# Performance work log

Hardware: AMD Instinct MI355X
Metric: run time of the kernel (lower is better)

## Reference

```python
import math
import jax, jax.numpy as jnp
import numpy as np

B, T, E = 2, 2048, 1024
H, KV = 16, 4
D = E // H          # 64
G = H // KV         # 4 groups


def rotate_half(x):
    x1, x2 = jnp.split(x, 2, axis=-1)
    return jnp.concatenate([-x2, x1], axis=-1)


def setup_inputs() -> dict:
    key = jax.random.key(0)
    ks = jax.random.split(key, 12)
    query = jax.random.normal(ks[0], (B, T, E), jnp.float32)
    key_t = jax.random.normal(ks[1], (B, T, E), jnp.float32)
    value = jax.random.normal(ks[2], (B, T, E), jnp.float32)
    # RoPE tables: [T, D]
    inv_freq = 1.0 / (10000.0 ** (np.arange(0, D, 2, dtype=np.float32) / D))
    pos = np.arange(T, dtype=np.float32)
    freqs = np.outer(pos, inv_freq)                      # [T, D/2]
    emb = np.concatenate([freqs, freqs], axis=-1)        # [T, D]
    cos_emb = jnp.asarray(np.cos(emb), jnp.float32)
    sin_emb = jnp.asarray(np.sin(emb), jnp.float32)
    # causal mask [1,1,T,T], True = keep
    mask = jnp.tril(jnp.ones((T, T), bool))[None, None, :, :]
    s = 0.02
    Wq = jax.random.normal(ks[3], (E, H * D), jnp.float32) * s
    bq = jnp.zeros((H * D,), jnp.float32)
    Wk = jax.random.normal(ks[4], (E, KV * D), jnp.float32) * s
    bk = jnp.zeros((KV * D,), jnp.float32)
    Wv = jax.random.normal(ks[5], (E, KV * D), jnp.float32) * s
    bv = jnp.zeros((KV * D,), jnp.float32)
    Wo = jax.random.normal(ks[6], (E, E), jnp.float32) * s
    bo = jnp.zeros((E,), jnp.float32)
    return {"query": query, "key": key_t, "value": value,
            "cos_emb": cos_emb, "sin_emb": sin_emb, "mask": mask,
            "Wq": Wq, "bq": bq, "Wk": Wk, "bk": bk,
            "Wv": Wv, "bv": bv, "Wo": Wo, "bo": bo}


def reference(query, key, value, cos_emb, sin_emb, mask,
              Wq, bq, Wk, bk, Wv, bv, Wo, bo):
    Bq, Tq, _ = query.shape
    Tk = key.shape[1]
    q = (query @ Wq + bq).reshape(Bq, Tq, H, D)          # [B,Tq,H,D]
    k = (key @ Wk + bk).reshape(Bq, Tk, KV, D)           # [B,Tk,KV,D]
    v = (value @ Wv + bv).reshape(Bq, Tk, KV, D)
    # expand kv heads across groups (head h = kv*G + g, consecutive repeat)
    k = jnp.repeat(k, G, axis=2)                         # [B,Tk,H,D]
    v = jnp.repeat(v, G, axis=2)
    # RoPE (applied post-expansion, as in the original)
    cos = cos_emb[None, :, None, :]                      # [1,T,1,D]
    sin = sin_emb[None, :, None, :]
    q = q * cos[:, :Tq] + rotate_half(q) * sin[:, :Tq]
    k = k * cos[:, :Tk] + rotate_half(k) * sin[:, :Tk]
    scores = jnp.einsum('bqhd,bkhd->bhqk', q, k) / math.sqrt(D)
    scores = jnp.where(mask[:, :, :Tq, :Tk], scores, jnp.float32(-jnp.inf))
    probs = jax.nn.softmax(scores, axis=-1)              # [B,H,Tq,Tk]
    attn = jnp.einsum('bhqk,bkhd->bqhd', probs, v).reshape(Bq, Tq, E)
    return attn @ Wo + bo
```

## Files before the change

kernel.cpp:

```cpp
#include <hip/hip_runtime.h>
#include <hip/hip_bf16.h>

constexpr int Bc  = 2;
constexpr int Tc  = 2048;
constexpr int Ec  = 1024;
constexpr int Hc  = 16;
constexpr int KVc = 4;
constexpr int Dc  = 64;

typedef short bf16x8 __attribute__((ext_vector_type(8)));
typedef short short4v __attribute__((ext_vector_type(4)));
typedef float f32x4  __attribute__((ext_vector_type(4)));
typedef float f32x16 __attribute__((ext_vector_type(16)));
typedef int   i32x4  __attribute__((ext_vector_type(4)));

__device__ inline short f2bf_bits(float f) {
    union { __hip_bfloat16 h; short s; } u;
    u.h = __float2bfloat16(f);
    return u.s;
}

__device__ inline float bf2f(short s) {
    union { short s16; __hip_bfloat16 h; } u;
    u.s16 = s;
    return __bfloat162float(u.h);
}

__device__ inline unsigned pkbf(float a, float b) {
    union { __hip_bfloat162 h2; unsigned u; } u;
    u.h2 = __float22bfloat162_rn(float2{a, b});
    return u.u;
}

__device__ inline float fexp2(float x) { return __builtin_exp2f(x); }

__device__ inline void permswap(unsigned &a, unsigned &b) {
    asm volatile("v_permlane32_swap_b32 %0, %1" : "+v"(a), "+v"(b));
}

__device__ inline void gload16(const short* g, short* lds) {
    __builtin_amdgcn_global_load_lds(
        (const __attribute__((address_space(1))) unsigned int*)g,
        (__attribute__((address_space(3))) unsigned int*)lds,
        16, 0, 0);
}

__global__ __launch_bounds__(256) void conv3_f32_bf16(
    const float* __restrict__ q, const float* __restrict__ k,
    const float* __restrict__ v,
    short* __restrict__ Xq, short* __restrict__ Xk, short* __restrict__ Xv)
{
    const int range = blockIdx.x >> 12;
    const int sub   = blockIdx.x & 4095;
    const float* x = range == 0 ? q : (range == 1 ? k : v);
    short*       y = range == 0 ? Xq : (range == 1 ? Xk : Xv);
    int i = (sub * 256 + threadIdx.x) * 4;
    float4 vv = *reinterpret_cast<const float4*>(x + i);
    short4v o;
    o[0] = f2bf_bits(vv.x);
    o[1] = f2bf_bits(vv.y);
    o[2] = f2bf_bits(vv.z);
    o[3] = f2bf_bits(vv.w);
    *reinterpret_cast<short4v*>(y + i) = o;
}

__global__ __launch_bounds__(256) void transp_all(
    const float* __restrict__ Wq, const float* __restrict__ Wk,
    const float* __restrict__ Wv, const float* __restrict__ Wo,
    short* __restrict__ Wqt, short* __restrict__ Wkt,
    short* __restrict__ Wvt, short* __restrict__ Wot)
{
    __shared__ float tile[32][33];
    const int id = blockIdx.x;
    const float* W; short* Wt; int N, bx, by;
    if (id < 1024)      { W = Wq; Wt = Wqt; N = 1024; bx = id & 31;          by = id >> 5; }
    else if (id < 1280) { W = Wk; Wt = Wkt; N = 256;  bx = (id - 1024) & 7;  by = (id - 1024) >> 3; }
    else if (id < 1536) { W = Wv; Wt = Wvt; N = 256;  bx = (id - 1280) & 7;  by = (id - 1280) >> 3; }
    else                { W = Wo; Wt = Wot; N = 1024; bx = (id - 1536) & 31; by = (id - 1536) >> 5; }
    const int K = 1024;
    int nb = bx * 32, kb = by * 32;
    int tx = threadIdx.x & 31, ty = threadIdx.x >> 5;
    #pragma unroll
    for (int j = 0; j < 4; ++j)
        tile[ty + j * 8][tx] = W[(size_t)(kb + ty + j * 8) * N + nb + tx];
    __syncthreads();
    #pragma unroll
    for (int j = 0; j < 4; ++j)
        Wt[(size_t)(nb + ty + j * 8) * K + kb + tx] = f2bf_bits(tile[tx][ty + j * 8]);
}

#define GEMM_CORE(A_, Bt_, Kdim_)                                              \
    const int lane = threadIdx.x & 63;                                         \
    const int w    = threadIdx.x >> 6;                                         \
    const int wm   = w >> 1, wn = w & 1;                                       \
    const int rin  = lane >> 3;                                                \
    const int swc  = ((lane & 7) ^ rin) * 8;                                   \
    f32x4 acc[4][2] = {};                                                      \
    for (int k0 = 0; k0 < (Kdim_); k0 += 64) {                                 \
        _Pragma("unroll")                                                      \
        for (int i2 = 0; i2 < 4; ++i2) {                                       \
            const int r = w * 32 + i2 * 8;                                     \
            gload16((A_) + (size_t)(m0 + r + rin) * (Kdim_) + k0 + swc,        \
                    As + r * 64);                                              \
        }                                                                      \
        _Pragma("unroll")                                                      \
        for (int i2 = 0; i2 < 2; ++i2) {                                       \
            const int r = w * 16 + i2 * 8;                                     \
            gload16((Bt_) + (size_t)(n0 + r + rin) * (Kdim_) + k0 + swc,       \
                    Bs + r * 64);                                              \
        }                                                                      \
        __syncthreads();                                                       \
        _Pragma("unroll")                                                      \
        for (int ks = 0; ks < 2; ++ks) {                                       \
            bf16x8 af[4], bfr[2];                                              \
            _Pragma("unroll")                                                  \
            for (int mi = 0; mi < 4; ++mi) {                                   \
                int row = wm * 64 + mi * 16 + (lane & 15);                     \
                int sl  = (ks * 4 + (lane >> 4)) ^ (row & 7);                  \
                af[mi] = *reinterpret_cast<const bf16x8*>(As + row * 64 + sl * 8); \
            }                                                                  \
            _Pragma("unroll")                                                  \
            for (int ni = 0; ni < 2; ++ni) {                                   \
                int row = wn * 32 + ni * 16 + (lane & 15);                     \
                int sl  = (ks * 4 + (lane >> 4)) ^ (row & 7);                  \
                bfr[ni] = *reinterpret_cast<const bf16x8*>(Bs + row * 64 + sl * 8); \
            }                                                                  \
            _Pragma("unroll")                                                  \
            for (int mi = 0; mi < 4; ++mi)                                     \
                _Pragma("unroll")                                              \
                for (int ni = 0; ni < 2; ++ni)                                 \
                    acc[mi][ni] = __builtin_amdgcn_mfma_f32_16x16x32_bf16(     \
                        af[mi], bfr[ni], acc[mi][ni], 0, 0, 0);                \
        }                                                                      \
        __syncthreads();                                                       \
    }

__global__ __launch_bounds__(256) void gemm_qkv(
    const short* __restrict__ Xq, const short* __restrict__ Xk,
    const short* __restrict__ Xv,
    const short* __restrict__ Wqt, const short* __restrict__ Wkt,
    const short* __restrict__ Wvt,
    const float* __restrict__ bq, const float* __restrict__ bk,
    const float* __restrict__ bv,
    short* __restrict__ Qp, short* __restrict__ Kp, short* __restrict__ VTp)
{
    __shared__ short As[128 * 64];
    __shared__ short Bs[64 * 64];
    const int gid = blockIdx.x;
    const short *A, *Bt; const float* bias; int bx, by, mode;
    if (gid < 512)      { mode = 0; A = Xq; Bt = Wqt; bias = bq; bx = gid & 15;         by = gid >> 4; }
    else if (gid < 640) { mode = 1; A = Xk; Bt = Wkt; bias = bk; bx = (gid - 512) & 3;  by = (gid - 512) >> 2; }
    else                { mode = 2; A = Xv; Bt = Wvt; bias = bv; bx = (gid - 640) & 3;  by = (gid - 640) >> 2; }
    const int m0 = by * 128, n0 = bx * 64;

    GEMM_CORE(A, Bt, 1024)

    #pragma unroll
    for (int mi = 0; mi < 4; ++mi)
        #pragma unroll
        for (int ni = 0; ni < 2; ++ni) {
            int col = n0 + wn * 32 + ni * 16 + (lane & 15);
            float bv2 = bias[col];
            #pragma unroll
            for (int i = 0; i < 4; ++i) {
                int row = m0 + wm * 64 + mi * 16 + ((lane >> 4) * 4) + i;
                float v = acc[mi][ni][i] + bv2;
                if (mode == 0)
                    Qp[(size_t)row * 1024 + col] = f2bf_bits(v);
                else if (mode == 1)
                    Kp[(size_t)row * 256 + col] = f2bf_bits(v);
                else
                    VTp[(((size_t)(row >> 11) * 256 + col) << 11) + (row & 2047)]
                        = f2bf_bits(v);
            }
        }
}

__global__ __launch_bounds__(256) void gemm_o(
    const short* __restrict__ A, const short* __restrict__ Bt,
    const float* __restrict__ bias, float* __restrict__ C)
{
    __shared__ short As[128 * 64];
    __shared__ short Bs[64 * 64];
    const int m0 = blockIdx.y * 128, n0 = blockIdx.x * 64;

    GEMM_CORE(A, Bt, 1024)

    #pragma unroll
    for (int mi = 0; mi < 4; ++mi)
        #pragma unroll
        for (int ni = 0; ni < 2; ++ni) {
            int col = n0 + wn * 32 + ni * 16 + (lane & 15);
            float bv2 = bias[col];
            #pragma unroll
            for (int i = 0; i < 4; ++i) {
                int row = m0 + wm * 64 + mi * 16 + ((lane >> 4) * 4) + i;
                C[(size_t)row * 1024 + col] = acc[mi][ni][i] + bv2;
            }
        }
}

__global__ __launch_bounds__(256) void rope_merged(
    short* __restrict__ Qp, short* __restrict__ Kp,
    const float* __restrict__ cosE, const float* __restrict__ sinE)
{
    short* x; int hbits; float scale; int idx;
    if (blockIdx.x < 2048) {
        x = Qp; hbits = 4; scale = 0.125f * 1.44269504089f;
        idx = blockIdx.x * 256 + threadIdx.x;
    } else {
        x = Kp; hbits = 2; scale = 1.0f;
        idx = (blockIdx.x - 2048) * 256 + threadIdx.x;
    }
    int dq  = (idx & 7) * 4;
    int hh  = (idx >> 3) & ((1 << hbits) - 1);
    int row = idx >> (3 + hbits);
    int t   = row & (Tc - 1);
    float4 c4 = *reinterpret_cast<const float4*>(cosE + t * 64 + dq);
    float4 s4 = *reinterpret_cast<const float4*>(sinE + t * 64 + dq);
    size_t base = (size_t)row * (64 << hbits) + hh * 64 + dq;
    short4v a = *reinterpret_cast<const short4v*>(x + base);
    short4v b = *reinterpret_cast<const short4v*>(x + base + 32);
    short4v oa, ob;
    float c[4] = {c4.x, c4.y, c4.z, c4.w};
    float s[4] = {s4.x, s4.y, s4.z, s4.w};
    #pragma unroll
    for (int j = 0; j < 4; ++j) {
        float x1 = bf2f(a[j]), x2 = bf2f(b[j]);
        oa[j] = f2bf_bits((x1 * c[j] - x2 * s[j]) * scale);
        ob[j] = f2bf_bits((x2 * c[j] + x1 * s[j]) * scale);
    }
    *reinterpret_cast<short4v*>(x + base)      = oa;
    *reinterpret_cast<short4v*>(x + base + 32) = ob;
}

__global__ __launch_bounds__(256, 3) void flash_gqa8(
    const short* __restrict__ Q,
    const short* __restrict__ Kx,
    const short* __restrict__ VT,
    short* __restrict__ attn,
    short* __restrict__ PO,
    float* __restrict__ ML)
{
    __shared__ short smem[16384];

    const int lane = threadIdx.x & 63;
    const int w    = threadIdx.x >> 6;
    const int lo   = lane & 31;
    const int hi   = lane >> 5;

    const int L   = blockIdx.x;
    const int xcd = L & 7;
    const int j   = L >> 3;
    const int g   = j & 3;
    const int u   = 39 - (j >> 2);
    int qt = 0, rem = u;
    while (true) { int nc0 = (qt >> 2) + 1; if (rem < nc0) break; rem -= nc0; ++qt; }
    const int c  = rem;
    const int nc = (qt >> 2) + 1;
    const int b   = xcd >> 2;
    const int kvh = xcd & 3;
    const int h   = kvh * 4 + g;
    const int slot = (b * 16 + h) * 40 + u;

    const int q0w = qt * 128 + w * 32;
    const int qg  = q0w + lo;

    bf16x8 qf[4];
    {
        const short* qp = Q + (size_t)(b * Tc + qg) * Ec + h * 64 + hi * 8;
        #pragma unroll
        for (int ds = 0; ds < 4; ++ds)
            qf[ds] = *reinterpret_cast<const bf16x8*>(qp + 16 * ds);
    }
    const short* Kb = Kx + (size_t)b * Tc * (KVc * Dc) + kvh * 64;
    const short* Vb = VT + (size_t)(b * KVc + kvh) * 64 * Tc;

    const int rin = lane >> 3;
    const int swc = ((lane & 7) ^ rin) * 8;
    auto stage = [&](int bufi, int kb2) {
        #pragma unroll
        for (int i2 = 0; i2 < 2; ++i2) {
            const int row = w * 16 + i2 * 8;
            gload16(Kb + (size_t)(kb2 + row + rin) * 256 + swc,
                    smem + bufi * 4096 + row * 64);
            gload16(Vb + (size_t)(row + rin) * Tc + kb2 + swc,
                    smem + 8192 + bufi * 4096 + row * 64);
        }
    };

    int slot8[4];
    #pragma unroll
    for (int i = 0; i < 4; ++i)
        slot8[i] = (((2 * i + hi) ^ (lo & 7)) * 8) + lo * 64;

    const int t0 = c * 8;
    const int t1 = min(c * 8 + 8, 2 * qt + 2);
    stage(0, t0 * 64);

    float m = -1e30f, l = 0.f;
    f32x16 o0 = {}, o1 = {};
    const int kv_hi = q0w + 32;

    for (int t = t0; t < t1; ++t) {
        const int kb  = t * 64;
        const int cur = (t - t0) & 1;
        asm volatile("s_waitcnt vmcnt(0)" ::: "memory");
        __builtin_amdgcn_s_barrier();
        if (t + 1 < t1) stage(cur ^ 1, kb + 64);

        if (kb < kv_hi) {
            const short* Kl = smem + cur * 4096;
            const short* Vl = Kl + 8192;

            bf16x8 kf0[4], kf1[4];
            #pragma unroll
            for (int ds = 0; ds < 4; ++ds) {
                kf0[ds] = *reinterpret_cast<const bf16x8*>(Kl + slot8[ds]);
                kf1[ds] = *reinterpret_cast<const bf16x8*>(Kl + slot8[ds] + 2048);
            }

            f32x16 s0 = {}, s1 = {};
            __builtin_amdgcn_s_setprio(1);
            #pragma unroll
            for (int ds = 0; ds < 4; ++ds) {
                s0 = __builtin_amdgcn_mfma_f32_32x32x16_bf16(kf0[ds], qf[ds], s0, 0, 0, 0);
                s1 = __builtin_amdgcn_mfma_f32_32x32x16_bf16(kf1[ds], qf[ds], s1, 0, 0, 0);
            }
            __builtin_amdgcn_s_setprio(0);

            bf16x8 vf0[4], vf1[4];
            #pragma unroll
            for (int sl = 0; sl < 4; ++sl) {
                vf0[sl] = *reinterpret_cast<const bf16x8*>(Vl + slot8[sl]);
                vf1[sl] = *reinterpret_cast<const bf16x8*>(Vl + slot8[sl] + 2048);
            }

            if (kb + 63 > q0w) {
                #pragma unroll
                for (int r = 0; r < 16; ++r) {
                    int kkl = (r & 3) + 8 * (r >> 2) + 4 * hi;
                    if (kb + kkl > qg)      s0[r] = -1e30f;
                    if (kb + 32 + kkl > qg) s1[r] = -1e30f;
                }
            }

            float mx[8];
            #pragma unroll
            for (int j2 = 0; j2 < 8; ++j2)
                mx[j2] = fmaxf(fmaxf(s0[2 * j2], s0[2 * j2 + 1]),
                               fmaxf(s1[2 * j2], s1[2 * j2 + 1]));
            #pragma unroll
            for (int st = 4; st > 0; st >>= 1)
                #pragma unroll
                for (int j2 = 0; j2 < st; ++j2) mx[j2] = fmaxf(mx[j2], mx[j2 + st]);
            float pm = fmaxf(mx[0], __shfl_xor(mx[0], 32));

            float corr = 1.0f;
            if (__any(pm > m + 8.0f)) {
                float mn = fmaxf(m, pm);
                corr = fexp2(m - mn);
                m = mn;
                #pragma unroll
                for (int r = 0; r < 16; ++r) { o0[r] *= corr; o1[r] *= corr; }
            }
            float rs = 0.f;
            #pragma unroll
            for (int r = 0; r < 16; ++r) {
                s0[r] = fexp2(s0[r] - m);
                s1[r] = fexp2(s1[r] - m);
                rs += s0[r] + s1[r];
            }
            rs += __shfl_xor(rs, 32);
            l = l * corr + rs;

            #pragma unroll
            for (int t2 = 0; t2 < 2; ++t2) {
                const f32x16& sv = t2 ? s1 : s0;
                unsigned pw[8];
                #pragma unroll
                for (int j2 = 0; j2 < 8; ++j2)
                    pw[j2] = pkbf(sv[2 * j2], sv[2 * j2 + 1]);
                #pragma unroll
                for (int u2 = 0; u2 < 2; ++u2) {
                    permswap(pw[4 * u2 + 0], pw[4 * u2 + 2]);
                    permswap(pw[4 * u2 + 1], pw[4 * u2 + 3]);
                    union { unsigned u4[4]; bf16x8 v; } pf;
                    pf.u4[0] = pw[4 * u2 + 0];
                    pf.u4[1] = pw[4 * u2 + 1];
                    pf.u4[2] = pw[4 * u2 + 2];
                    pf.u4[3] = pw[4 * u2 + 3];
                    int sl = 2 * t2 + u2;
                    __builtin_amdgcn_s_setprio(1);
                    o0 = __builtin_amdgcn_mfma_f32_32x32x16_bf16(vf0[sl], pf.v, o0, 0, 0, 0);
                    o1 = __builtin_amdgcn_mfma_f32_32x32x16_bf16(vf1[sl], pf.v, o1, 0, 0, 0);
                    __builtin_amdgcn_s_setprio(0);
                }
            }
        }
    }
    __builtin_amdgcn_s_barrier();

    const float inv = (nc == 1) ? (1.0f / l) : 1.0f;
    short* ob = smem + w * 2048;
    #pragma unroll
    for (int r = 0; r < 16; ++r) {
        int d0 = (r & 3) + 8 * (r >> 2) + 4 * hi;
        ob[lo * 64 + ( d0       ^ ((lo & 7) << 3))] = f2bf_bits(o0[r] * inv);
        ob[lo * 64 + ((d0 + 32) ^ ((lo & 7) << 3))] = f2bf_bits(o1[r] * inv);
    }
    if (nc > 1 && hi == 0) {
        ML[(size_t)slot * 256 + (w * 32 + lo) * 2]     = m;
        ML[(size_t)slot * 256 + (w * 32 + lo) * 2 + 1] = l;
    }
    #pragma unroll
    for (int j2 = 0; j2 < 4; ++j2) {
        int row = lane >> 1;
        int c8  = ((lane & 1) * 4 + j2) * 8;
        bf16x8 v = *reinterpret_cast<const bf16x8*>(
            ob + row * 64 + (c8 ^ ((row & 7) << 3)));
        if (nc == 1)
            *reinterpret_cast<bf16x8*>(
                attn + (size_t)(b * Tc + q0w + row) * Ec + h * 64 + c8) = v;
        else
            *reinterpret_cast<bf16x8*>(
                PO + (size_t)slot * 8192 + (w * 32 + row) * 64 + c8) = v;
    }
}

__global__ __launch_bounds__(256) void combine_kernel(
    const short* __restrict__ PO, const float* __restrict__ ML,
    short* __restrict__ attn)
{
    const int qt    = 4 + (blockIdx.x >> 2);
    const int rg    = blockIdx.x & 3;
    const int combo = blockIdx.y;
    const int h = combo & 15, b = combo >> 4;
    const int nc = (qt >> 2) + 1;
    const int k  = qt >> 2, r4 = qt & 3;
    const int base = (k + 1) * (2 * k + r4);
    const int slot0 = combo * 40 + base;

    const int r  = rg * 32 + (threadIdx.x >> 3);
    const int d8 = (threadIdx.x & 7) * 8;

    float mv[4], lv[4];
    float M = -1e30f;
    #pragma unroll 4
    for (int cc = 0; cc < nc; ++cc) {
        mv[cc] = ML[(size_t)(slot0 + cc) * 256 + r * 2];
        lv[cc] = ML[(size_t)(slot0 + cc) * 256 + r * 2 + 1];
        M = fmaxf(M, mv[cc]);
    }
    float Lsum = 0.f;
    float a[8] = {};
    #pragma unroll 4
    for (int cc = 0; cc < nc; ++cc) {
        float wgt = fexp2(mv[cc] - M);
        Lsum += wgt * lv[cc];
        bf16x8 po = *reinterpret_cast<const bf16x8*>(
            PO + (size_t)(slot0 + cc) * 8192 + r * 64 + d8);
        #pragma unroll
        for (int j = 0; j < 8; ++j) a[j] += wgt * bf2f(po[j]);
    }
    float inv = 1.0f / Lsum;
    bf16x8 o;
    #pragma unroll
    for (int j = 0; j < 8; ++j) o[j] = f2bf_bits(a[j] * inv);
    *reinterpret_cast<bf16x8*>(
        attn + (size_t)(b * Tc + qt * 128 + r) * Ec + h * 64 + d8) = o;
}

extern "C" void kernel_launch(void* const* d_in, const int* in_sizes, int n_in,
                              void* d_out, int out_size, void* d_ws, size_t ws_size,
                              hipStream_t stream)
{
    const float* query = (const float*)d_in[0];
    const float* key   = (const float*)d_in[1];
    const float* value = (const float*)d_in[2];
    const float* cosE  = (const float*)d_in[3];
    const float* sinE  = (const float*)d_in[4];
    const float* Wq = (const float*)d_in[6];
    const float* bq = (const float*)d_in[7];
    const float* Wk = (const float*)d_in[8];
    const float* bk = (const float*)d_in[9];
    const float* Wv = (const float*)d_in[10];
    const float* bv = (const float*)d_in[11];
    const float* Wo = (const float*)d_in[12];
    const float* bo = (const float*)d_in[13];

    char* ws = (char*)d_ws;
    constexpr size_t MB = 1u << 20;
    short* Xq   = (short*)(ws + 0);
    short* Xk   = (short*)(ws + 8  * MB);
    short* Xv   = (short*)(ws + 16 * MB);
    short* Wqt  = (short*)(ws + 24 * MB);
    short* Wkt  = (short*)(ws + 26 * MB);
    short* Wvt  = (short*)(ws + 26 * MB + 512 * 1024);
    short* Wot  = (short*)(ws + 27 * MB);
    short* Qp   = (short*)(ws + 29 * MB);
    short* Kp   = (short*)(ws + 37 * MB);
    short* VTp  = (short*)(ws + 39 * MB);
    short* attn = (short*)(ws + 41 * MB);
    short* PO   = (short*)(ws + 0);
    float* ML   = (float*)(ws + 21 * MB);
    (void)ws_size;

    conv3_f32_bf16<<<12288, 256, 0, stream>>>(query, key, value, Xq, Xk, Xv);
    transp_all<<<2560, 256, 0, stream>>>(Wq, Wk, Wv, Wo, Wqt, Wkt, Wvt, Wot);
    gemm_qkv<<<768, 256, 0, stream>>>(Xq, Xk, Xv, Wqt, Wkt, Wvt,
                                      bq, bk, bv, Qp, Kp, VTp);
    rope_merged<<<2560, 256, 0, stream>>>(Qp, Kp, cosE, sinE);
    flash_gqa8<<<1280, 256, 0, stream>>>(Qp, Kp, VTp, attn, PO, ML);
    combine_kernel<<<dim3(48, 32), 256, 0, stream>>>(PO, ML, attn);
    gemm_o<<<dim3(16, 32), 256, 0, stream>>>(attn, Wot, bo, (float*)d_out);
}
```

Before: 120.0 us.

## Fuse fp32-to-bf16 input conversion into QKV GEMM and Q RoPE into attention

Removes the standalone fp32-to-bf16 conversion kernel. The QKV GEMM now loads fp32 activations directly, converts them in registers and stores them swizzled into LDS. Q's RoPE and softmax scaling move into the flash attention kernel's Q-fragment load, so the separate RoPE kernel now rotates only K. This cuts a launch and a round trip of the activations through global memory. In exchange, the GEMM's A loads become synchronous register loads instead of direct-to-LDS async loads, and the attention prologue does more work.

```diff
diff --git a/kernel.cpp b/kernel.cpp
--- a/kernel.cpp
+++ b/kernel.cpp
@@ -43,25 +43,6 @@
         (const __attribute__((address_space(1))) unsigned int*)g,
         (__attribute__((address_space(3))) unsigned int*)lds,
         16, 0, 0);
-}
-
-__global__ __launch_bounds__(256) void conv3_f32_bf16(
-    const float* __restrict__ q, const float* __restrict__ k,
-    const float* __restrict__ v,
-    short* __restrict__ Xq, short* __restrict__ Xk, short* __restrict__ Xv)
-{
-    const int range = blockIdx.x >> 12;
-    const int sub   = blockIdx.x & 4095;
-    const float* x = range == 0 ? q : (range == 1 ? k : v);
-    short*       y = range == 0 ? Xq : (range == 1 ? Xk : Xv);
-    int i = (sub * 256 + threadIdx.x) * 4;
-    float4 vv = *reinterpret_cast<const float4*>(x + i);
-    short4v o;
-    o[0] = f2bf_bits(vv.x);
-    o[1] = f2bf_bits(vv.y);
-    o[2] = f2bf_bits(vv.z);
-    o[3] = f2bf_bits(vv.w);
-    *reinterpret_cast<short4v*>(y + i) = o;
 }
 
 __global__ __launch_bounds__(256) void transp_all(
@@ -89,55 +70,9 @@
         Wt[(size_t)(nb + ty + j * 8) * K + kb + tx] = f2bf_bits(tile[tx][ty + j * 8]);
 }
 
-#define GEMM_CORE(A_, Bt_, Kdim_)                                              \
-    const int lane = threadIdx.x & 63;                                         \
-    const int w    = threadIdx.x >> 6;                                         \
-    const int wm   = w >> 1, wn = w & 1;                                       \
-    const int rin  = lane >> 3;                                                \
-    const int swc  = ((lane & 7) ^ rin) * 8;                                   \
-    f32x4 acc[4][2] = {};                                                      \
-    for (int k0 = 0; k0 < (Kdim_); k0 += 64) {                                 \
-        _Pragma("unroll")                                                      \
-        for (int i2 = 0; i2 < 4; ++i2) {                                       \
-            const int r = w * 32 + i2 * 8;                                     \
-            gload16((A_) + (size_t)(m0 + r + rin) * (Kdim_) + k0 + swc,        \
-                    As + r * 64);                                              \
-        }                                                                      \
-        _Pragma("unroll")                                                      \
-        for (int i2 = 0; i2 < 2; ++i2) {                                       \
-            const int r = w * 16 + i2 * 8;                                     \
-            gload16((Bt_) + (size_t)(n0 + r + rin) * (Kdim_) + k0 + swc,       \
-                    Bs + r * 64);                                              \
-        }                                                                      \
-        __syncthreads();                                                       \
-        _Pragma("unroll")                                                      \
-        for (int ks = 0; ks < 2; ++ks) {                                       \
-            bf16x8 af[4], bfr[2];                                              \
-            _Pragma("unroll")                                                  \
-            for (int mi = 0; mi < 4; ++mi) {                                   \
-                int row = wm * 64 + mi * 16 + (lane & 15);                     \
-                int sl  = (ks * 4 + (lane >> 4)) ^ (row & 7);                  \
-                af[mi] = *reinterpret_cast<const bf16x8*>(As + row * 64 + sl * 8); \
-            }                                                                  \
-            _Pragma("unroll")                                                  \
-            for (int ni = 0; ni < 2; ++ni) {                                   \
-                int row = wn * 32 + ni * 16 + (lane & 15);                     \
-                int sl  = (ks * 4 + (lane >> 4)) ^ (row & 7);                  \
-                bfr[ni] = *reinterpret_cast<const bf16x8*>(Bs + row * 64 + sl * 8); \
-            }                                                                  \
-            _Pragma("unroll")                                                  \
-            for (int mi = 0; mi < 4; ++mi)                                     \
-                _Pragma("unroll")                                              \
-                for (int ni = 0; ni < 2; ++ni)                                 \
-                    acc[mi][ni] = __builtin_amdgcn_mfma_f32_16x16x32_bf16(     \
-                        af[mi], bfr[ni], acc[mi][ni], 0, 0, 0);                \
-        }                                                                      \
-        __syncthreads();                                                       \
-    }
-
 __global__ __launch_bounds__(256) void gemm_qkv(
-    const short* __restrict__ Xq, const short* __restrict__ Xk,
-    const short* __restrict__ Xv,
+    const float* __restrict__ Xq, const float* __restrict__ Xk,
+    const float* __restrict__ Xv,
     const short* __restrict__ Wqt, const short* __restrict__ Wkt,
     const short* __restrict__ Wvt,
     const float* __restrict__ bq, const float* __restrict__ bk,
@@ -147,13 +82,66 @@
     __shared__ short As[128 * 64];
     __shared__ short Bs[64 * 64];
     const int gid = blockIdx.x;
-    const short *A, *Bt; const float* bias; int bx, by, mode;
+    const float* A; const short* Bt; const float* bias; int bx, by, mode;
     if (gid < 512)      { mode = 0; A = Xq; Bt = Wqt; bias = bq; bx = gid & 15;         by = gid >> 4; }
     else if (gid < 640) { mode = 1; A = Xk; Bt = Wkt; bias = bk; bx = (gid - 512) & 3;  by = (gid - 512) >> 2; }
     else                { mode = 2; A = Xv; Bt = Wvt; bias = bv; bx = (gid - 640) & 3;  by = (gid - 640) >> 2; }
     const int m0 = by * 128, n0 = bx * 64;
 
-    GEMM_CORE(A, Bt, 1024)
+    const int lane = threadIdx.x & 63;
+    const int w    = threadIdx.x >> 6;
+    const int wm   = w >> 1, wn = w & 1;
+    const int rin  = lane >> 3;
+    const int swc  = ((lane & 7) ^ rin) * 8;
+
+    f32x4 acc[4][2] = {};
+
+    for (int k0 = 0; k0 < 1024; k0 += 64) {
+        #pragma unroll
+        for (int it = 0; it < 4; ++it) {
+            int s   = threadIdx.x + it * 256;
+            int row = s >> 3;
+            int c8  = s & 7;
+            const float* src = A + (size_t)(m0 + row) * 1024 + k0 + c8 * 8;
+            float4 f0 = *reinterpret_cast<const float4*>(src);
+            float4 f1 = *reinterpret_cast<const float4*>(src + 4);
+            union { unsigned u4[4]; bf16x8 v; } pk;
+            pk.u4[0] = pkbf(f0.x, f0.y);
+            pk.u4[1] = pkbf(f0.z, f0.w);
+            pk.u4[2] = pkbf(f1.x, f1.y);
+            pk.u4[3] = pkbf(f1.z, f1.w);
+            *reinterpret_cast<bf16x8*>(As + row * 64 + ((c8 ^ (row & 7)) * 8)) = pk.v;
+        }
+        #pragma unroll
+        for (int i2 = 0; i2 < 2; ++i2) {
+            const int r = w * 16 + i2 * 8;
+            gload16(Bt + (size_t)(n0 + r + rin) * 1024 + k0 + swc, Bs + r * 64);
+        }
+        __syncthreads();
+        #pragma unroll
+        for (int ks = 0; ks < 2; ++ks) {
+            bf16x8 af[4], bfr[2];
+            #pragma unroll
+            for (int mi = 0; mi < 4; ++mi) {
+                int row = wm * 64 + mi * 16 + (lane & 15);
+                int sl  = (ks * 4 + (lane >> 4)) ^ (row & 7);
+                af[mi] = *reinterpret_cast<const bf16x8*>(As + row * 64 + sl * 8);
+            }
+            #pragma unroll
+            for (int ni = 0; ni < 2; ++ni) {
+                int row = wn * 32 + ni * 16 + (lane & 15);
+                int sl  = (ks * 4 + (lane >> 4)) ^ (row & 7);
+                bfr[ni] = *reinterpret_cast<const bf16x8*>(Bs + row * 64 + sl * 8);
+            }
+            #pragma unroll
+            for (int mi = 0; mi < 4; ++mi)
+                #pragma unroll
+                for (int ni = 0; ni < 2; ++ni)
+                    acc[mi][ni] = __builtin_amdgcn_mfma_f32_16x16x32_bf16(
+                        af[mi], bfr[ni], acc[mi][ni], 0, 0, 0);
+        }
+        __syncthreads();
+    }
 
     #pragma unroll
     for (int mi = 0; mi < 4; ++mi)
@@ -184,7 +172,50 @@
     __shared__ short Bs[64 * 64];
     const int m0 = blockIdx.y * 128, n0 = blockIdx.x * 64;
 
-    GEMM_CORE(A, Bt, 1024)
+    const int lane = threadIdx.x & 63;
+    const int w    = threadIdx.x >> 6;
+    const int wm   = w >> 1, wn = w & 1;
+    const int rin  = lane >> 3;
+    const int swc  = ((lane & 7) ^ rin) * 8;
+
+    f32x4 acc[4][2] = {};
+
+    for (int k0 = 0; k0 < 1024; k0 += 64) {
+        #pragma unroll
+        for (int i2 = 0; i2 < 4; ++i2) {
+            const int r = w * 32 + i2 * 8;
+            gload16(A + (size_t)(m0 + r + rin) * 1024 + k0 + swc, As + r * 64);
+        }
+        #pragma unroll
+        for (int i2 = 0; i2 < 2; ++i2) {
+            const int r = w * 16 + i2 * 8;
+            gload16(Bt + (size_t)(n0 + r + rin) * 1024 + k0 + swc, Bs + r * 64);
+        }
+        __syncthreads();
+        #pragma unroll
+        for (int ks = 0; ks < 2; ++ks) {
+            bf16x8 af[4], bfr[2];
+            #pragma unroll
+            for (int mi = 0; mi < 4; ++mi) {
+                int row = wm * 64 + mi * 16 + (lane & 15);
+                int sl  = (ks * 4 + (lane >> 4)) ^ (row & 7);
+                af[mi] = *reinterpret_cast<const bf16x8*>(As + row * 64 + sl * 8);
+            }
+            #pragma unroll
+            for (int ni = 0; ni < 2; ++ni) {
+                int row = wn * 32 + ni * 16 + (lane & 15);
+                int sl  = (ks * 4 + (lane >> 4)) ^ (row & 7);
+                bfr[ni] = *reinterpret_cast<const bf16x8*>(Bs + row * 64 + sl * 8);
+            }
+            #pragma unroll
+            for (int mi = 0; mi < 4; ++mi)
+                #pragma unroll
+                for (int ni = 0; ni < 2; ++ni)
+                    acc[mi][ni] = __builtin_amdgcn_mfma_f32_16x16x32_bf16(
+                        af[mi], bfr[ni], acc[mi][ni], 0, 0, 0);
+        }
+        __syncthreads();
+    }
 
     #pragma unroll
     for (int mi = 0; mi < 4; ++mi)
@@ -200,44 +231,39 @@
         }
 }
 
-__global__ __launch_bounds__(256) void rope_merged(
-    short* __restrict__ Qp, short* __restrict__ Kp,
+__global__ __launch_bounds__(256) void rope_k(
+    short* __restrict__ Kp,
     const float* __restrict__ cosE, const float* __restrict__ sinE)
 {
-    short* x; int hbits; float scale; int idx;
-    if (blockIdx.x < 2048) {
-        x = Qp; hbits = 4; scale = 0.125f * 1.44269504089f;
-        idx = blockIdx.x * 256 + threadIdx.x;
-    } else {
-        x = Kp; hbits = 2; scale = 1.0f;
-        idx = (blockIdx.x - 2048) * 256 + threadIdx.x;
-    }
+    int idx = blockIdx.x * 256 + threadIdx.x;
     int dq  = (idx & 7) * 4;
-    int hh  = (idx >> 3) & ((1 << hbits) - 1);
-    int row = idx >> (3 + hbits);
+    int hh  = (idx >> 3) & 3;
+    int row = idx >> 5;
     int t   = row & (Tc - 1);
     float4 c4 = *reinterpret_cast<const float4*>(cosE + t * 64 + dq);
     float4 s4 = *reinterpret_cast<const float4*>(sinE + t * 64 + dq);
-    size_t base = (size_t)row * (64 << hbits) + hh * 64 + dq;
-    short4v a = *reinterpret_cast<const short4v*>(x + base);
-    short4v b = *reinterpret_cast<const short4v*>(x + base + 32);
+    size_t base = (size_t)row * 256 + hh * 64 + dq;
+    short4v a = *reinterpret_cast<const short4v*>(Kp + base);
+    short4v b = *reinterpret_cast<const short4v*>(Kp + base + 32);
     short4v oa, ob;
     float c[4] = {c4.x, c4.y, c4.z, c4.w};
     float s[4] = {s4.x, s4.y, s4.z, s4.w};
     #pragma unroll
     for (int j = 0; j < 4; ++j) {
         float x1 = bf2f(a[j]), x2 = bf2f(b[j]);
-        oa[j] = f2bf_bits((x1 * c[j] - x2 * s[j]) * scale);
-        ob[j] = f2bf_bits((x2 * c[j] + x1 * s[j]) * scale);
-    }
-    *reinterpret_cast<short4v*>(x + base)      = oa;
-    *reinterpret_cast<short4v*>(x + base + 32) = ob;
-}
-
-__global__ __launch_bounds__(256, 3) void flash_gqa8(
+        oa[j] = f2bf_bits(x1 * c[j] - x2 * s[j]);
+        ob[j] = f2bf_bits(x2 * c[j] + x1 * s[j]);
+    }
+    *reinterpret_cast<short4v*>(Kp + base)      = oa;
+    *reinterpret_cast<short4v*>(Kp + base + 32) = ob;
+}
+
+__global__ __launch_bounds__(256, 3) void flash_gqa9(
     const short* __restrict__ Q,
     const short* __restrict__ Kx,
     const short* __restrict__ VT,
+    const float* __restrict__ cosE,
+    const float* __restrict__ sinE,
     short* __restrict__ attn,
     short* __restrict__ PO,
     float* __restrict__ ML)
@@ -269,9 +295,36 @@
     bf16x8 qf[4];
     {
         const short* qp = Q + (size_t)(b * Tc + qg) * Ec + h * 64 + hi * 8;
-        #pragma unroll
-        for (int ds = 0; ds < 4; ++ds)
-            qf[ds] = *reinterpret_cast<const bf16x8*>(qp + 16 * ds);
+        const float* ct = cosE + (size_t)qg * 64 + hi * 8;
+        const float* st = sinE + (size_t)qg * 64 + hi * 8;
+        float qv[4][8], cv[4][8], sv[4][8];
+        #pragma unroll
+        for (int ds = 0; ds < 4; ++ds) {
+            bf16x8 raw = *reinterpret_cast<const bf16x8*>(qp + 16 * ds);
+            float4 c0 = *reinterpret_cast<const float4*>(ct + 16 * ds);
+            float4 c1 = *reinterpret_cast<const float4*>(ct + 16 * ds + 4);
+            float4 s0 = *reinterpret_cast<const float4*>(st + 16 * ds);
+            float4 s1 = *reinterpret_cast<const float4*>(st + 16 * ds + 4);
+            #pragma unroll
+            for (int j2 = 0; j2 < 8; ++j2) qv[ds][j2] = bf2f(raw[j2]);
+            cv[ds][0] = c0.x; cv[ds][1] = c0.y; cv[ds][2] = c0.z; cv[ds][3] = c0.w;
+            cv[ds][4] = c1.x; cv[ds][5] = c1.y; cv[ds][6] = c1.z; cv[ds][7] = c1.w;
+            sv[ds][0] = s0.x; sv[ds][1] = s0.y; sv[ds][2] = s0.z; sv[ds][3] = s0.w;
+            sv[ds][4] = s1.x; sv[ds][5] = s1.y; sv[ds][6] = s1.z; sv[ds][7] = s1.w;
+        }
+        constexpr float SC = 0.125f * 1.44269504089f;
+        #pragma unroll
+        for (int ds = 0; ds < 2; ++ds) {
+            #pragma unroll
+            for (int j2 = 0; j2 < 8; j2 += 2) {
+                float a0 = (qv[ds][j2]     * cv[ds][j2]     - qv[ds+2][j2]     * sv[ds][j2])     * SC;
+                float a1 = (qv[ds][j2+1]   * cv[ds][j2+1]   - qv[ds+2][j2+1]   * sv[ds][j2+1])   * SC;
+                float b0 = (qv[ds+2][j2]   * cv[ds+2][j2]   + qv[ds][j2]       * sv[ds+2][j2])   * SC;
+                float b1 = (qv[ds+2][j2+1] * cv[ds+2][j2+1] + qv[ds][j2+1]     * sv[ds+2][j2+1]) * SC;
+                reinterpret_cast<unsigned*>(&qf[ds])[j2 >> 1]     = pkbf(a0, a1);
+                reinterpret_cast<unsigned*>(&qf[ds + 2])[j2 >> 1] = pkbf(b0, b1);
+            }
+        }
     }
     const short* Kb = Kx + (size_t)b * Tc * (KVc * Dc) + kvh * 64;
     const short* Vb = VT + (size_t)(b * KVc + kvh) * 64 * Tc;
@@ -376,11 +429,11 @@
 
             #pragma unroll
             for (int t2 = 0; t2 < 2; ++t2) {
-                const f32x16& sv = t2 ? s1 : s0;
+                const f32x16& sv2 = t2 ? s1 : s0;
                 unsigned pw[8];
                 #pragma unroll
                 for (int j2 = 0; j2 < 8; ++j2)
-                    pw[j2] = pkbf(sv[2 * j2], sv[2 * j2 + 1]);
+                    pw[j2] = pkbf(sv2[2 * j2], sv2[2 * j2 + 1]);
                 #pragma unroll
                 for (int u2 = 0; u2 < 2; ++u2) {
                     permswap(pw[4 * u2 + 0], pw[4 * u2 + 2]);
@@ -491,9 +544,8 @@
 
     char* ws = (char*)d_ws;
     constexpr size_t MB = 1u << 20;
-    short* Xq   = (short*)(ws + 0);
-    short* Xk   = (short*)(ws + 8  * MB);
-    short* Xv   = (short*)(ws + 16 * MB);
+    short* PO   = (short*)(ws + 0);
+    float* ML   = (float*)(ws + 21 * MB);
     short* Wqt  = (short*)(ws + 24 * MB);
     short* Wkt  = (short*)(ws + 26 * MB);
     short* Wvt  = (short*)(ws + 26 * MB + 512 * 1024);
@@ -502,16 +554,13 @@
     short* Kp   = (short*)(ws + 37 * MB);
     short* VTp  = (short*)(ws + 39 * MB);
     short* attn = (short*)(ws + 41 * MB);
-    short* PO   = (short*)(ws + 0);
-    float* ML   = (float*)(ws + 21 * MB);
     (void)ws_size;
 
-    conv3_f32_bf16<<<12288, 256, 0, stream>>>(query, key, value, Xq, Xk, Xv);
     transp_all<<<2560, 256, 0, stream>>>(Wq, Wk, Wv, Wo, Wqt, Wkt, Wvt, Wot);
-    gemm_qkv<<<768, 256, 0, stream>>>(Xq, Xk, Xv, Wqt, Wkt, Wvt,
+    gemm_qkv<<<768, 256, 0, stream>>>(query, key, value, Wqt, Wkt, Wvt,
                                       bq, bk, bv, Qp, Kp, VTp);
-    rope_merged<<<2560, 256, 0, stream>>>(Qp, Kp, cosE, sinE);
-    flash_gqa8<<<1280, 256, 0, stream>>>(Qp, Kp, VTp, attn, PO, ML);
+    rope_k<<<512, 256, 0, stream>>>(Kp, cosE, sinE);
+    flash_gqa9<<<1280, 256, 0, stream>>>(Qp, Kp, VTp, cosE, sinE, attn, PO, ML);
     combine_kernel<<<dim3(48, 32), 256, 0, stream>>>(PO, ML, attn);
     gemm_o<<<dim3(16, 32), 256, 0, stream>>>(attn, Wot, bo, (float*)d_out);
 }
```

Result: slower. 133.4 us, median of 2 (+11.2%).
